# Performance work log

Hardware: AMD Instinct MI355X
Metric: run time of the kernel (lower is better)

The kernel has to match this reference:

```python
import jax, jax.numpy as jnp
import numpy as np

HALF_HIDDEN = 64  # hidden_size // 2


def _lstm_scan(xs, W_ih, W_hh):
    # xs: [T, B, H]; returns final (h, c), each [B, half_hidden]
    B = xs.shape[1]
    h0 = jnp.zeros((B, HALF_HIDDEN), xs.dtype)
    c0 = jnp.zeros((B, HALF_HIDDEN), xs.dtype)

    def step(carry, x_t):
        h, c = carry
        gates = x_t @ W_ih.T + h @ W_hh.T          # [B, 4*hh]
        i_g, f_g, g_g, o_g = jnp.split(gates, 4, axis=1)
        c_new = jax.nn.sigmoid(f_g) * c + jax.nn.sigmoid(i_g) * jnp.tanh(g_g)
        h_new = jax.nn.sigmoid(o_g) * jnp.tanh(c_new)
        return (h_new, c_new), None

    (h, c), _ = jax.lax.scan(step, (h0, c0), xs)
    return h, c


def setup_inputs() -> dict:
    key = jax.random.key(0)
    ks = jax.random.split(key, 8)
    B, T, V, H, HH = 1024, 512, 128, 128, HALF_HIDDEN
    scale = 0.1
    return {
        "x": jax.random.randint(ks[0], (B, T), 0, V, dtype=jnp.int32),
        "lengths": jax.random.randint(ks[1], (B,), 1, T, dtype=jnp.int32),
        "emb": jax.random.normal(ks[2], (V, H), jnp.float32) * scale,
        "W_ih_f": jax.random.normal(ks[3], (4 * HH, H), jnp.float32) * scale,
        "W_hh_f": jax.random.normal(ks[4], (4 * HH, HH), jnp.float32) * scale,
        "W_ih_b": jax.random.normal(ks[5], (4 * HH, H), jnp.float32) * scale,
        "W_hh_b": jax.random.normal(ks[6], (4 * HH, HH), jnp.float32) * scale,
        "W_fc": jax.random.normal(ks[7], (V, H), jnp.float32) * scale,
        "b_fc": jnp.zeros((V,), jnp.float32),
    }


def reference(x, lengths, emb, W_ih_f, W_hh_f, W_ih_b, W_hh_b, W_fc, b_fc):
    # embedding lookup: [B, T, H] -> time-major [T, B, H]
    embedded = emb[x]
    xs = jnp.transpose(embedded, (1, 0, 2))
    h_f, _ = _lstm_scan(xs, W_ih_f, W_hh_f)            # forward direction
    h_b, _ = _lstm_scan(xs[::-1], W_ih_b, W_hh_b)      # backward direction
    hidden_cat = jnp.concatenate([h_f, h_b], axis=1)   # [B, hidden]
    return hidden_cat @ W_fc.T + b_fc                  # [B, vocab]
```

## Files before the change

kernel.cpp:

```cpp
#include <hip/hip_runtime.h>
#include <hip/hip_bf16.h>


#define T_STEPS 512
#define BATCH   1024
#define VOCAB   128
#define HID     128
#define HH      64
#define NG      256
#define MB      4
#define XPITCH  520

#define L2E  1.4426950408889634f
#define L2E2 2.8853900817779268f

typedef __attribute__((ext_vector_type(8))) short bf16x8;
typedef __attribute__((ext_vector_type(4))) float f32x4;
typedef unsigned int  u32;
typedef unsigned short u16;

__device__ __forceinline__ float sigmoid_f(float x) {
    return __builtin_amdgcn_rcpf(1.0f + __builtin_amdgcn_exp2f(-x * L2E));
}
__device__ __forceinline__ float tanh_f(float x) {
    return 1.0f - 2.0f * __builtin_amdgcn_rcpf(1.0f + __builtin_amdgcn_exp2f(x * L2E2));
}
__device__ __forceinline__ u16 f2bf_rne(float f) {
    u32 u = __builtin_bit_cast(u32, f);
    u += 0x7FFFu + ((u >> 16) & 1u);
    return (u16)(u >> 16);
}
__device__ __forceinline__ void barrier_lgkm() {
    asm volatile("s_waitcnt lgkmcnt(0)\n\ts_barrier" ::: "memory");
}

__global__ __launch_bounds__(256) void build_tab_kernel(
    const float* __restrict__ emb,
    const float* __restrict__ W_ih_f,
    const float* __restrict__ W_ih_b,
    const float* __restrict__ W_hh_f,
    const float* __restrict__ W_hh_b,
    float* __restrict__ tab3,
    u16*   __restrict__ whh_bf)
{
    int v = blockIdx.x, d = blockIdx.y, tid = threadIdx.x;
    int j = tid >> 2, g = tid & 3;
    int gr = g * HH + j;
    const float* W = d ? W_ih_b : W_ih_f;
    const float4* e4 = (const float4*)(emb + v * HID);
    const float4* w4 = (const float4*)(W + gr * HID);
    float acc = 0.0f;
#pragma unroll
    for (int k = 0; k < HID / 4; ++k) {
        float4 e = e4[k]; float4 w = w4[k];
        acc += e.x * w.x + e.y * w.y + e.z * w.z + e.w * w.w;
    }
    tab3[(d * VOCAB + v) * NG + j * 4 + g] = acc;

    if (tid < 128) {
        const float* Whh = d ? W_hh_b : W_hh_f;
        int idx = v * 128 + tid;
        whh_bf[d * NG * HH + idx] = f2bf_rne(Whh[idx]);
    }
}

__global__ __launch_bounds__(256, 2) void lstm_rec_kernel(
    const int*  __restrict__ x,
    const u16*  __restrict__ whh_bf,
    const float* __restrict__ tab3,
    float* __restrict__ hfin)
{
    __shared__ __align__(16) u32 xsT[MB][XPITCH];
    __shared__ __align__(16) u16 hbuf[2][MB][80];

    const int tid  = threadIdx.x;
    const int lane = tid & 63;
    const int wave = tid >> 6;
    const int quad = lane >> 4;
    const int m    = lane & 15;
    const int dir    = blockIdx.y;
    const int b_base = blockIdx.x * MB;

    for (int i = tid; i < MB * T_STEPS; i += 256) {
        int bl = i >> 9, t = i & (T_STEPS - 1);
        int ts = dir ? (T_STEPS - 1 - t) : t;
        xsT[bl][ts] = ((u32)x[(b_base + bl) * T_STEPS + t]) << 10;
    }
    if (tid < MB * 8)
        xsT[tid >> 3][T_STEPS + (tid & 7)] = 0;
    for (int i = tid; i < (int)(sizeof(hbuf) / 4); i += 256)
        ((u32*)hbuf)[i] = 0;

    const u16* WB = whh_bf + dir * NG * HH;
    bf16x8 Bg[4][2];
#pragma unroll
    for (int g = 0; g < 4; ++g)
#pragma unroll
        for (int kc = 0; kc < 2; ++kc)
            Bg[g][kc] = *(const bf16x8*)(WB + (g * HH + wave * 16 + m) * HH
                                            + kc * 32 + quad * 8);

    const char* tabB = (const char*)tab3 + (size_t)dir * VOCAB * NG * 4;
    const u32 joff = (u32)(wave * 16 + m) * 16u;
    const int aoff = (m >> 2) * 80 + quad * 8;
    const int woff = quad * 80 + wave * 16 + m;

    const f32x4 z4 = {0.f, 0.f, 0.f, 0.f};
    float cc = 0.f, hcur = 0.f;

    __syncthreads();

    int4 qA = *(const int4*)&xsT[quad][0];
    int4 qB = *(const int4*)&xsT[quad][4];
    float4 X0 = *(const float4*)(tabB + (u32)qA.x + joff);
    float4 X1;

    auto stepf = [&](int p, const float4 Xc, float4& Xn, u32 e) {
        __builtin_amdgcn_s_setprio(1);
        const u16* rh = &hbuf[p][0][0];
        u16* wh = &hbuf[p ^ 1][0][0];
        bf16x8 Ah0 = *(const bf16x8*)(rh + aoff);
        bf16x8 Ah1 = *(const bf16x8*)(rh + aoff + 32);

        Xn = *(const float4*)(tabB + e + joff);

        f32x4 aI = __builtin_amdgcn_mfma_f32_16x16x32_bf16(Ah0, Bg[0][0], z4, 0, 0, 0);
        f32x4 aF = __builtin_amdgcn_mfma_f32_16x16x32_bf16(Ah0, Bg[1][0], z4, 0, 0, 0);
        f32x4 aG = __builtin_amdgcn_mfma_f32_16x16x32_bf16(Ah0, Bg[2][0], z4, 0, 0, 0);
        f32x4 aO = __builtin_amdgcn_mfma_f32_16x16x32_bf16(Ah0, Bg[3][0], z4, 0, 0, 0);
        aI = __builtin_amdgcn_mfma_f32_16x16x32_bf16(Ah1, Bg[0][1], aI, 0, 0, 0);
        aF = __builtin_amdgcn_mfma_f32_16x16x32_bf16(Ah1, Bg[1][1], aF, 0, 0, 0);
        aG = __builtin_amdgcn_mfma_f32_16x16x32_bf16(Ah1, Bg[2][1], aG, 0, 0, 0);
        aO = __builtin_amdgcn_mfma_f32_16x16x32_bf16(Ah1, Bg[3][1], aO, 0, 0, 0);

        float gi = aI[0] + Xc.x;
        float gf = aF[0] + Xc.y;
        float gg = aG[0] + Xc.z;
        float go = aO[0] + Xc.w;
        __builtin_amdgcn_s_setprio(0);

        cc   = sigmoid_f(gf) * cc + sigmoid_f(gi) * tanh_f(gg);
        hcur = sigmoid_f(go) * tanh_f(cc);

        u32 hb;
        asm("v_cvt_pk_bf16_f32 %0, %1, %2" : "=v"(hb) : "v"(hcur), "v"(hcur));
        wh[woff] = (u16)hb;

        barrier_lgkm();
    };

    for (int kk = 0; kk < T_STEPS / 8; ++kk) {
        stepf(0, X0, X1, (u32)qA.y);
        stepf(1, X1, X0, (u32)qA.z);
        stepf(0, X0, X1, (u32)qA.w);
        qA = *(const int4*)&xsT[quad][8 * kk + 8];
        stepf(1, X1, X0, (u32)qB.x);
        stepf(0, X0, X1, (u32)qB.y);
        stepf(1, X1, X0, (u32)qB.z);
        stepf(0, X0, X1, (u32)qB.w);
        qB = *(const int4*)&xsT[quad][8 * kk + 12];
        stepf(1, X1, X0, (u32)qA.x);
    }

    hfin[(dir * BATCH + b_base + quad) * HH + wave * 16 + m] = hcur;
}

__global__ __launch_bounds__(256) void fc_kernel(
    const float* __restrict__ hfin,
    const float* __restrict__ W_fc,
    const float* __restrict__ b_fc,
    float* __restrict__ out)
{
    __shared__ float wfc[HID * 129];
    __shared__ float hid[8][HID];
    const int tid = threadIdx.x;
    const int b0  = blockIdx.x * 8;

    for (int i = tid; i < HID * HID; i += 256) {
        int r = i >> 7, c = i & 127;
        wfc[r * 129 + c] = W_fc[i];
    }
    for (int i = tid; i < 8 * HID; i += 256) {
        int bb = i >> 7, v = i & 127;
        hid[bb][v] = (v < HH) ? hfin[(0 * BATCH + b0 + bb) * HH + v]
                              : hfin[(1 * BATCH + b0 + bb) * HH + (v - HH)];
    }
    __syncthreads();

    const int v  = tid & 127;
    const int bs = (tid >> 7) * 4;
    const float bias = b_fc[v];
    const float* wrow = wfc + v * 129;
#pragma unroll
    for (int r = 0; r < 4; ++r) {
        const float* h = hid[bs + r];
        float acc = bias;
#pragma unroll
        for (int k = 0; k < HID; k += 4) {
            acc += wrow[k]     * h[k]     + wrow[k + 1] * h[k + 1]
                 + wrow[k + 2] * h[k + 2] + wrow[k + 3] * h[k + 3];
        }
        out[(b0 + bs + r) * HID + v] = acc;
    }
}

extern "C" void kernel_launch(void* const* d_in, const int* in_sizes, int n_in,
                              void* d_out, int out_size, void* d_ws, size_t ws_size,
                              hipStream_t stream) {
    const int*   x      = (const int*)d_in[0];
    const float* emb    = (const float*)d_in[2];
    const float* W_ih_f = (const float*)d_in[3];
    const float* W_hh_f = (const float*)d_in[4];
    const float* W_ih_b = (const float*)d_in[5];
    const float* W_hh_b = (const float*)d_in[6];
    const float* W_fc   = (const float*)d_in[7];
    const float* b_fc   = (const float*)d_in[8];
    float* out = (float*)d_out;

    float* tab3   = (float*)d_ws;
    u16*   whh_bf = (u16*)(tab3 + 2 * VOCAB * NG);
    float* hfin   = (float*)(whh_bf + 2 * NG * HH);

    build_tab_kernel<<<dim3(VOCAB, 2), 256, 0, stream>>>(
        emb, W_ih_f, W_ih_b, W_hh_f, W_hh_b, tab3, whh_bf);
    lstm_rec_kernel<<<dim3(BATCH / MB, 2), 256, 0, stream>>>(x, whh_bf, tab3, hfin);
    fc_kernel<<<dim3(BATCH / 8), 256, 0, stream>>>(hfin, W_fc, b_fc, out);
}
```

Before: 214.4 us.

## Make each wave own whole batch rows and drop per-step block barriers

Restructures the LSTM recurrence so each wave holds all 64 hidden units for its own batch rows. Each wave computes the full 4x64 gate matrix with replicated W_hh fragments and rebuilds its MFMA A operand from register state via DPP swaps and ds_bpermute. This removes the LDS hidden-state double buffer and the workgroup barrier on every timestep, and doubles batch rows per block to 8. The cost is 4x more MFMA work per wave (mostly redundant, since only 16 rows are live), far more registers for B fragments (occupancy drops to 1 block per SIMD group), and half the blocks.

```diff
diff --git a/kernel.cpp b/kernel.cpp
--- a/kernel.cpp
+++ b/kernel.cpp
@@ -8,7 +8,6 @@
 #define HID     128
 #define HH      64
 #define NG      256
-#define MB      4
 #define XPITCH  520
 
 #define L2E  1.4426950408889634f
@@ -16,6 +15,7 @@
 
 typedef __attribute__((ext_vector_type(8))) short bf16x8;
 typedef __attribute__((ext_vector_type(4))) float f32x4;
+typedef __attribute__((ext_vector_type(4))) int   i32x4;
 typedef unsigned int  u32;
 typedef unsigned short u16;
 
@@ -30,8 +30,10 @@
     u += 0x7FFFu + ((u >> 16) & 1u);
     return (u16)(u >> 16);
 }
-__device__ __forceinline__ void barrier_lgkm() {
-    asm volatile("s_waitcnt lgkmcnt(0)\n\ts_barrier" ::: "memory");
+__device__ __forceinline__ float dpp_swap1(float v) {
+    int i = __builtin_bit_cast(int, v);
+    i = __builtin_amdgcn_mov_dpp(i, 0xB1, 0xF, 0xF, true);
+    return __builtin_bit_cast(float, i);
 }
 
 __global__ __launch_bounds__(256) void build_tab_kernel(
@@ -64,105 +66,130 @@
     }
 }
 
-__global__ __launch_bounds__(256, 2) void lstm_rec_kernel(
+__global__ __launch_bounds__(256, 1) void lstm_rec_kernel(
     const int*  __restrict__ x,
     const u16*  __restrict__ whh_bf,
     const float* __restrict__ tab3,
     float* __restrict__ hfin)
 {
-    __shared__ __align__(16) u32 xsT[MB][XPITCH];
-    __shared__ __align__(16) u16 hbuf[2][MB][80];
+    __shared__ __align__(16) u32 xsT[8][XPITCH];
 
     const int tid  = threadIdx.x;
     const int lane = tid & 63;
     const int wave = tid >> 6;
-    const int quad = lane >> 4;
+    const int q    = lane >> 4;
     const int m    = lane & 15;
     const int dir    = blockIdx.y;
-    const int b_base = blockIdx.x * MB;
-
-    for (int i = tid; i < MB * T_STEPS; i += 256) {
+    const int b_base = blockIdx.x * 8;
+
+    for (int i = tid; i < 8 * T_STEPS; i += 256) {
         int bl = i >> 9, t = i & (T_STEPS - 1);
         int ts = dir ? (T_STEPS - 1 - t) : t;
         xsT[bl][ts] = ((u32)x[(b_base + bl) * T_STEPS + t]) << 10;
     }
-    if (tid < MB * 8)
+    if (tid < 64)
         xsT[tid >> 3][T_STEPS + (tid & 7)] = 0;
-    for (int i = tid; i < (int)(sizeof(hbuf) / 4); i += 256)
-        ((u32*)hbuf)[i] = 0;
 
     const u16* WB = whh_bf + dir * NG * HH;
-    bf16x8 Bg[4][2];
+    bf16x8 Bg[4][4][2];
 #pragma unroll
     for (int g = 0; g < 4; ++g)
 #pragma unroll
-        for (int kc = 0; kc < 2; ++kc)
-            Bg[g][kc] = *(const bf16x8*)(WB + (g * HH + wave * 16 + m) * HH
-                                            + kc * 32 + quad * 8);
+        for (int n = 0; n < 4; ++n)
+#pragma unroll
+            for (int c = 0; c < 2; ++c)
+                Bg[g][n][c] = *(const bf16x8*)(WB + (g * 64 + n * 16 + m) * HH
+                                                  + c * 32 + q * 8);
 
     const char* tabB = (const char*)tab3 + (size_t)dir * VOCAB * NG * 4;
-    const u32 joff = (u32)(wave * 16 + m) * 16u;
-    const int aoff = (m >> 2) * 80 + quad * 8;
-    const int woff = quad * 80 + wave * 16 + m;
+    const int r     = lane >> 5;
+    const int j0    = lane & 31;
+    const u32 joff  = (u32)j0 << 4;
+    const int myrow = wave * 2 + r;
+    const int addrB = ((m >> 3) << 7) | (q << 5);
 
     const f32x4 z4 = {0.f, 0.f, 0.f, 0.f};
-    float cc = 0.f, hcur = 0.f;
+    float cc0 = 0.f, cc1 = 0.f, h0 = 0.f, h1 = 0.f;
 
     __syncthreads();
 
-    int4 qA = *(const int4*)&xsT[quad][0];
-    int4 qB = *(const int4*)&xsT[quad][4];
-    float4 X0 = *(const float4*)(tabB + (u32)qA.x + joff);
-    float4 X1;
-
-    auto stepf = [&](int p, const float4 Xc, float4& Xn, u32 e) {
-        __builtin_amdgcn_s_setprio(1);
-        const u16* rh = &hbuf[p][0][0];
-        u16* wh = &hbuf[p ^ 1][0][0];
-        bf16x8 Ah0 = *(const bf16x8*)(rh + aoff);
-        bf16x8 Ah1 = *(const bf16x8*)(rh + aoff + 32);
-
-        Xn = *(const float4*)(tabB + e + joff);
-
-        f32x4 aI = __builtin_amdgcn_mfma_f32_16x16x32_bf16(Ah0, Bg[0][0], z4, 0, 0, 0);
-        f32x4 aF = __builtin_amdgcn_mfma_f32_16x16x32_bf16(Ah0, Bg[1][0], z4, 0, 0, 0);
-        f32x4 aG = __builtin_amdgcn_mfma_f32_16x16x32_bf16(Ah0, Bg[2][0], z4, 0, 0, 0);
-        f32x4 aO = __builtin_amdgcn_mfma_f32_16x16x32_bf16(Ah0, Bg[3][0], z4, 0, 0, 0);
-        aI = __builtin_amdgcn_mfma_f32_16x16x32_bf16(Ah1, Bg[0][1], aI, 0, 0, 0);
-        aF = __builtin_amdgcn_mfma_f32_16x16x32_bf16(Ah1, Bg[1][1], aF, 0, 0, 0);
-        aG = __builtin_amdgcn_mfma_f32_16x16x32_bf16(Ah1, Bg[2][1], aG, 0, 0, 0);
-        aO = __builtin_amdgcn_mfma_f32_16x16x32_bf16(Ah1, Bg[3][1], aO, 0, 0, 0);
-
-        float gi = aI[0] + Xc.x;
-        float gf = aF[0] + Xc.y;
-        float gg = aG[0] + Xc.z;
-        float go = aO[0] + Xc.w;
-        __builtin_amdgcn_s_setprio(0);
-
-        cc   = sigmoid_f(gf) * cc + sigmoid_f(gi) * tanh_f(gg);
-        hcur = sigmoid_f(go) * tanh_f(cc);
-
-        u32 hb;
-        asm("v_cvt_pk_bf16_f32 %0, %1, %2" : "=v"(hb) : "v"(hcur), "v"(hcur));
-        wh[woff] = (u16)hb;
-
-        barrier_lgkm();
+    int4 qA = *(const int4*)&xsT[myrow][0];
+    int4 qB = *(const int4*)&xsT[myrow][4];
+    float4 XA0 = *(const float4*)(tabB + (u32)qA.x + joff);
+    float4 XA1 = *(const float4*)(tabB + (u32)qA.x + joff + 512);
+    float4 XB0, XB1;
+
+    auto stepf = [&](const float4 Xc0, const float4 Xc1,
+                     float4& Xn0, float4& Xn1, u32 e) {
+        float h0n = dpp_swap1(h0);
+        float h1n = dpp_swap1(h1);
+        u32 P0, P1;
+        asm("v_cvt_pk_bf16_f32 %0, %1, %2" : "=v"(P0) : "v"(h0), "v"(h0n));
+        asm("v_cvt_pk_bf16_f32 %0, %1, %2" : "=v"(P1) : "v"(h1), "v"(h1n));
+        int a0 = __builtin_amdgcn_ds_bpermute(addrB,      __builtin_bit_cast(int, P0));
+        int a1 = __builtin_amdgcn_ds_bpermute(addrB + 8,  __builtin_bit_cast(int, P0));
+        int a2 = __builtin_amdgcn_ds_bpermute(addrB + 16, __builtin_bit_cast(int, P0));
+        int a3 = __builtin_amdgcn_ds_bpermute(addrB + 24, __builtin_bit_cast(int, P0));
+        int b0 = __builtin_amdgcn_ds_bpermute(addrB,      __builtin_bit_cast(int, P1));
+        int b1 = __builtin_amdgcn_ds_bpermute(addrB + 8,  __builtin_bit_cast(int, P1));
+        int b2 = __builtin_amdgcn_ds_bpermute(addrB + 16, __builtin_bit_cast(int, P1));
+        int b3 = __builtin_amdgcn_ds_bpermute(addrB + 24, __builtin_bit_cast(int, P1));
+        i32x4 va = {a0, a1, a2, a3};
+        i32x4 vb = {b0, b1, b2, b3};
+        bf16x8 A0 = __builtin_bit_cast(bf16x8, va);
+        bf16x8 A1 = __builtin_bit_cast(bf16x8, vb);
+
+        Xn0 = *(const float4*)(tabB + e + joff);
+        Xn1 = *(const float4*)(tabB + e + joff + 512);
+
+        f32x4 acc[4][4];
+#pragma unroll
+        for (int g = 0; g < 4; ++g)
+#pragma unroll
+            for (int n = 0; n < 4; ++n)
+                acc[g][n] = __builtin_amdgcn_mfma_f32_16x16x32_bf16(
+                    A0, Bg[g][n][0], z4, 0, 0, 0);
+#pragma unroll
+        for (int g = 0; g < 4; ++g)
+#pragma unroll
+            for (int n = 0; n < 4; ++n)
+                acc[g][n] = __builtin_amdgcn_mfma_f32_16x16x32_bf16(
+                    A1, Bg[g][n][1], acc[g][n], 0, 0, 0);
+
+        const bool s = (q & 1);
+        float gi0 = (s ? acc[0][1][0] : acc[0][0][0]) + Xc0.x;
+        float gf0 = (s ? acc[1][1][0] : acc[1][0][0]) + Xc0.y;
+        float gg0 = (s ? acc[2][1][0] : acc[2][0][0]) + Xc0.z;
+        float go0 = (s ? acc[3][1][0] : acc[3][0][0]) + Xc0.w;
+        float gi1 = (s ? acc[0][3][0] : acc[0][2][0]) + Xc1.x;
+        float gf1 = (s ? acc[1][3][0] : acc[1][2][0]) + Xc1.y;
+        float gg1 = (s ? acc[2][3][0] : acc[2][2][0]) + Xc1.z;
+        float go1 = (s ? acc[3][3][0] : acc[3][2][0]) + Xc1.w;
+
+        cc0 = sigmoid_f(gf0) * cc0 + sigmoid_f(gi0) * tanh_f(gg0);
+        h0  = sigmoid_f(go0) * tanh_f(cc0);
+        cc1 = sigmoid_f(gf1) * cc1 + sigmoid_f(gi1) * tanh_f(gg1);
+        h1  = sigmoid_f(go1) * tanh_f(cc1);
     };
 
     for (int kk = 0; kk < T_STEPS / 8; ++kk) {
-        stepf(0, X0, X1, (u32)qA.y);
-        stepf(1, X1, X0, (u32)qA.z);
-        stepf(0, X0, X1, (u32)qA.w);
-        qA = *(const int4*)&xsT[quad][8 * kk + 8];
-        stepf(1, X1, X0, (u32)qB.x);
-        stepf(0, X0, X1, (u32)qB.y);
-        stepf(1, X1, X0, (u32)qB.z);
-        stepf(0, X0, X1, (u32)qB.w);
-        qB = *(const int4*)&xsT[quad][8 * kk + 12];
-        stepf(1, X1, X0, (u32)qA.x);
-    }
-
-    hfin[(dir * BATCH + b_base + quad) * HH + wave * 16 + m] = hcur;
+        stepf(XA0, XA1, XB0, XB1, (u32)qA.y);
+        stepf(XB0, XB1, XA0, XA1, (u32)qA.z);
+        stepf(XA0, XA1, XB0, XB1, (u32)qA.w);
+        qA = *(const int4*)&xsT[myrow][8 * kk + 8];
+        stepf(XB0, XB1, XA0, XA1, (u32)qB.x);
+        stepf(XA0, XA1, XB0, XB1, (u32)qB.y);
+        stepf(XB0, XB1, XA0, XA1, (u32)qB.z);
+        stepf(XA0, XA1, XB0, XB1, (u32)qB.w);
+        qB = *(const int4*)&xsT[myrow][8 * kk + 12];
+        stepf(XB0, XB1, XA0, XA1, (u32)qA.x);
+    }
+
+    {
+        float* dst = hfin + ((size_t)dir * BATCH + b_base + myrow) * HH;
+        dst[j0]      = h0;
+        dst[j0 + 32] = h1;
+    }
 }
 
 __global__ __launch_bounds__(256) void fc_kernel(
@@ -223,6 +250,6 @@
 
     build_tab_kernel<<<dim3(VOCAB, 2), 256, 0, stream>>>(
         emb, W_ih_f, W_ih_b, W_hh_f, W_hh_b, tab3, whh_bf);
-    lstm_rec_kernel<<<dim3(BATCH / MB, 2), 256, 0, stream>>>(x, whh_bf, tab3, hfin);
+    lstm_rec_kernel<<<dim3(BATCH / 8, 2), 256, 0, stream>>>(x, whh_bf, tab3, hfin);
     fc_kernel<<<dim3(BATCH / 8), 256, 0, stream>>>(hfin, W_fc, b_fc, out);
 }
```

Measured after the change: 344.1 us. 60.5% more time.

## Halve batch rows per block and give each wave 32 hidden units

Applied to the files above, without the earlier changes.

Reduces the recurrent block from four waves over four batch rows to two waves over two batch rows. Each wave now computes two 16-column MFMA tiles per gate, covering 32 hidden units, and selects its result by lane group. The intent is a cheaper two-wave barrier and more independent blocks to hide latency. The cost is double the MFMAs per wave per step on the serial recurrence path, and more redundant rows in the MFMA A operand.

```diff
diff --git a/kernel.cpp b/kernel.cpp
--- a/kernel.cpp
+++ b/kernel.cpp
@@ -8,7 +8,7 @@
 #define HID     128
 #define HH      64
 #define NG      256
-#define MB      4
+#define MB      2
 #define XPITCH  520
 
 #define L2E  1.4426950408889634f
@@ -64,7 +64,7 @@
     }
 }
 
-__global__ __launch_bounds__(256, 2) void lstm_rec_kernel(
+__global__ __launch_bounds__(128, 2) void lstm_rec_kernel(
     const int*  __restrict__ x,
     const u16*  __restrict__ whh_bf,
     const float* __restrict__ tab3,
@@ -76,42 +76,46 @@
     const int tid  = threadIdx.x;
     const int lane = tid & 63;
     const int wave = tid >> 6;
-    const int quad = lane >> 4;
+    const int q    = lane >> 4;
     const int m    = lane & 15;
     const int dir    = blockIdx.y;
     const int b_base = blockIdx.x * MB;
 
-    for (int i = tid; i < MB * T_STEPS; i += 256) {
+    for (int i = tid; i < MB * T_STEPS; i += 128) {
         int bl = i >> 9, t = i & (T_STEPS - 1);
         int ts = dir ? (T_STEPS - 1 - t) : t;
         xsT[bl][ts] = ((u32)x[(b_base + bl) * T_STEPS + t]) << 10;
     }
     if (tid < MB * 8)
         xsT[tid >> 3][T_STEPS + (tid & 7)] = 0;
-    for (int i = tid; i < (int)(sizeof(hbuf) / 4); i += 256)
+    for (int i = tid; i < (int)(sizeof(hbuf) / 4); i += 128)
         ((u32*)hbuf)[i] = 0;
 
     const u16* WB = whh_bf + dir * NG * HH;
-    bf16x8 Bg[4][2];
+    bf16x8 Bg[4][2][2];
 #pragma unroll
     for (int g = 0; g < 4; ++g)
 #pragma unroll
-        for (int kc = 0; kc < 2; ++kc)
-            Bg[g][kc] = *(const bf16x8*)(WB + (g * HH + wave * 16 + m) * HH
-                                            + kc * 32 + quad * 8);
+        for (int n = 0; n < 2; ++n)
+#pragma unroll
+            for (int c = 0; c < 2; ++c)
+                Bg[g][n][c] = *(const bf16x8*)(
+                    WB + (g * 64 + wave * 32 + n * 16 + m) * HH + c * 32 + q * 8);
 
     const char* tabB = (const char*)tab3 + (size_t)dir * VOCAB * NG * 4;
-    const u32 joff = (u32)(wave * 16 + m) * 16u;
-    const int aoff = (m >> 2) * 80 + quad * 8;
-    const int woff = quad * 80 + wave * 16 + m;
+    const int r    = q >> 1;
+    const int jj   = wave * 32 + (q & 1) * 16 + m;
+    const u32 joff = (u32)jj << 4;
+    const int aoff = (m >> 3) * 80 + q * 8;
+    const int woff = r * 80 + jj;
 
     const f32x4 z4 = {0.f, 0.f, 0.f, 0.f};
     float cc = 0.f, hcur = 0.f;
 
     __syncthreads();
 
-    int4 qA = *(const int4*)&xsT[quad][0];
-    int4 qB = *(const int4*)&xsT[quad][4];
+    int4 qA = *(const int4*)&xsT[r][0];
+    int4 qB = *(const int4*)&xsT[r][4];
     float4 X0 = *(const float4*)(tabB + (u32)qA.x + joff);
     float4 X1;
 
@@ -124,19 +128,25 @@
 
         Xn = *(const float4*)(tabB + e + joff);
 
-        f32x4 aI = __builtin_amdgcn_mfma_f32_16x16x32_bf16(Ah0, Bg[0][0], z4, 0, 0, 0);
-        f32x4 aF = __builtin_amdgcn_mfma_f32_16x16x32_bf16(Ah0, Bg[1][0], z4, 0, 0, 0);
-        f32x4 aG = __builtin_amdgcn_mfma_f32_16x16x32_bf16(Ah0, Bg[2][0], z4, 0, 0, 0);
-        f32x4 aO = __builtin_amdgcn_mfma_f32_16x16x32_bf16(Ah0, Bg[3][0], z4, 0, 0, 0);
-        aI = __builtin_amdgcn_mfma_f32_16x16x32_bf16(Ah1, Bg[0][1], aI, 0, 0, 0);
-        aF = __builtin_amdgcn_mfma_f32_16x16x32_bf16(Ah1, Bg[1][1], aF, 0, 0, 0);
-        aG = __builtin_amdgcn_mfma_f32_16x16x32_bf16(Ah1, Bg[2][1], aG, 0, 0, 0);
-        aO = __builtin_amdgcn_mfma_f32_16x16x32_bf16(Ah1, Bg[3][1], aO, 0, 0, 0);
-
-        float gi = aI[0] + Xc.x;
-        float gf = aF[0] + Xc.y;
-        float gg = aG[0] + Xc.z;
-        float go = aO[0] + Xc.w;
+        f32x4 acc[4][2];
+#pragma unroll
+        for (int g = 0; g < 4; ++g)
+#pragma unroll
+            for (int n = 0; n < 2; ++n)
+                acc[g][n] = __builtin_amdgcn_mfma_f32_16x16x32_bf16(
+                    Ah0, Bg[g][n][0], z4, 0, 0, 0);
+#pragma unroll
+        for (int g = 0; g < 4; ++g)
+#pragma unroll
+            for (int n = 0; n < 2; ++n)
+                acc[g][n] = __builtin_amdgcn_mfma_f32_16x16x32_bf16(
+                    Ah1, Bg[g][n][1], acc[g][n], 0, 0, 0);
+
+        const bool s = (q & 1);
+        float gi = (s ? acc[0][1][0] : acc[0][0][0]) + Xc.x;
+        float gf = (s ? acc[1][1][0] : acc[1][0][0]) + Xc.y;
+        float gg = (s ? acc[2][1][0] : acc[2][0][0]) + Xc.z;
+        float go = (s ? acc[3][1][0] : acc[3][0][0]) + Xc.w;
         __builtin_amdgcn_s_setprio(0);
 
         cc   = sigmoid_f(gf) * cc + sigmoid_f(gi) * tanh_f(gg);
@@ -153,16 +163,16 @@
         stepf(0, X0, X1, (u32)qA.y);
         stepf(1, X1, X0, (u32)qA.z);
         stepf(0, X0, X1, (u32)qA.w);
-        qA = *(const int4*)&xsT[quad][8 * kk + 8];
+        qA = *(const int4*)&xsT[r][8 * kk + 8];
         stepf(1, X1, X0, (u32)qB.x);
         stepf(0, X0, X1, (u32)qB.y);
         stepf(1, X1, X0, (u32)qB.z);
         stepf(0, X0, X1, (u32)qB.w);
-        qB = *(const int4*)&xsT[quad][8 * kk + 12];
+        qB = *(const int4*)&xsT[r][8 * kk + 12];
         stepf(1, X1, X0, (u32)qA.x);
     }
 
-    hfin[(dir * BATCH + b_base + quad) * HH + wave * 16 + m] = hcur;
+    hfin[(dir * BATCH + b_base + r) * HH + jj] = hcur;
 }
 
 __global__ __launch_bounds__(256) void fc_kernel(
@@ -223,6 +233,6 @@
 
     build_tab_kernel<<<dim3(VOCAB, 2), 256, 0, stream>>>(
         emb, W_ih_f, W_ih_b, W_hh_f, W_hh_b, tab3, whh_bf);
-    lstm_rec_kernel<<<dim3(BATCH / MB, 2), 256, 0, stream>>>(x, whh_bf, tab3, hfin);
+    lstm_rec_kernel<<<dim3(BATCH / MB, 2), 128, 0, stream>>>(x, whh_bf, tab3, hfin);
     fc_kernel<<<dim3(BATCH / 8), 256, 0, stream>>>(hfin, W_fc, b_fc, out);
 }
```

After: 278.4 us. 29.9% more time.

## Fuse final FC projection into LSTM kernel via atomic partial sums, drop setprio

Applied to the files above, without the earlier changes.

Removes the separate fc_kernel. Each recurrence block writes its final hidden state to shared memory and computes its direction's half of the output projection, which it adds into the output with atomicAdd. The output is zeroed with a memset first, and only the forward-direction blocks add the bias. The s_setprio hints around the MFMA section are also removed. This saves one kernel launch and the hfin round trip through global memory, at the cost of an extra memset, atomics, and fp32 addition order that is no longer deterministic.

```diff
diff --git a/kernel.cpp b/kernel.cpp
--- a/kernel.cpp
+++ b/kernel.cpp
@@ -68,7 +68,9 @@
     const int*  __restrict__ x,
     const u16*  __restrict__ whh_bf,
     const float* __restrict__ tab3,
-    float* __restrict__ hfin)
+    const float* __restrict__ W_fc,
+    const float* __restrict__ b_fc,
+    float* __restrict__ out)
 {
     __shared__ __align__(16) u32 xsT[MB][XPITCH];
     __shared__ __align__(16) u16 hbuf[2][MB][80];
@@ -116,7 +118,6 @@
     float4 X1;
 
     auto stepf = [&](int p, const float4 Xc, float4& Xn, u32 e) {
-        __builtin_amdgcn_s_setprio(1);
         const u16* rh = &hbuf[p][0][0];
         u16* wh = &hbuf[p ^ 1][0][0];
         bf16x8 Ah0 = *(const bf16x8*)(rh + aoff);
@@ -137,7 +138,6 @@
         float gf = aF[0] + Xc.y;
         float gg = aG[0] + Xc.z;
         float go = aO[0] + Xc.w;
-        __builtin_amdgcn_s_setprio(0);
 
         cc   = sigmoid_f(gf) * cc + sigmoid_f(gi) * tanh_f(gg);
         hcur = sigmoid_f(go) * tanh_f(cc);
@@ -162,45 +162,34 @@
         stepf(1, X1, X0, (u32)qA.x);
     }
 
-    hfin[(dir * BATCH + b_base + quad) * HH + wave * 16 + m] = hcur;
-}
-
-__global__ __launch_bounds__(256) void fc_kernel(
-    const float* __restrict__ hfin,
-    const float* __restrict__ W_fc,
-    const float* __restrict__ b_fc,
-    float* __restrict__ out)
-{
-    __shared__ float wfc[HID * 129];
-    __shared__ float hid[8][HID];
-    const int tid = threadIdx.x;
-    const int b0  = blockIdx.x * 8;
-
-    for (int i = tid; i < HID * HID; i += 256) {
-        int r = i >> 7, c = i & 127;
-        wfc[r * 129 + c] = W_fc[i];
-    }
-    for (int i = tid; i < 8 * HID; i += 256) {
-        int bb = i >> 7, v = i & 127;
-        hid[bb][v] = (v < HH) ? hfin[(0 * BATCH + b0 + bb) * HH + v]
-                              : hfin[(1 * BATCH + b0 + bb) * HH + (v - HH)];
-    }
+    float* hs = (float*)&xsT[0][0];
+    hs[quad * HH + wave * 16 + m] = hcur;
     __syncthreads();
 
-    const int v  = tid & 127;
-    const int bs = (tid >> 7) * 4;
-    const float bias = b_fc[v];
-    const float* wrow = wfc + v * 129;
-#pragma unroll
-    for (int r = 0; r < 4; ++r) {
-        const float* h = hid[bs + r];
-        float acc = bias;
-#pragma unroll
-        for (int k = 0; k < HID; k += 4) {
-            acc += wrow[k]     * h[k]     + wrow[k + 1] * h[k + 1]
-                 + wrow[k + 2] * h[k + 2] + wrow[k + 3] * h[k + 3];
+    {
+        const int v  = tid & 127;
+        const int rp = tid >> 7;
+        const int r0 = 2 * rp, r1 = 2 * rp + 1;
+        const float* wv = W_fc + v * HID + dir * HH;
+        const float4* w4 = (const float4*)wv;
+        const float4* h4a = (const float4*)(hs + r0 * HH);
+        const float4* h4b = (const float4*)(hs + r1 * HH);
+        float acc0 = 0.f, acc1 = 0.f;
+#pragma unroll
+        for (int k = 0; k < HH / 4; ++k) {
+            float4 w = w4[k];
+            float4 a = h4a[k];
+            float4 b = h4b[k];
+            acc0 += w.x * a.x + w.y * a.y + w.z * a.z + w.w * a.w;
+            acc1 += w.x * b.x + w.y * b.y + w.z * b.z + w.w * b.w;
         }
-        out[(b0 + bs + r) * HID + v] = acc;
+        if (dir == 0) {
+            float bias = b_fc[v];
+            acc0 += bias;
+            acc1 += bias;
+        }
+        atomicAdd(&out[(b_base + r0) * HID + v], acc0);
+        atomicAdd(&out[(b_base + r1) * HID + v], acc1);
     }
 }
 
@@ -219,10 +208,10 @@
 
     float* tab3   = (float*)d_ws;
     u16*   whh_bf = (u16*)(tab3 + 2 * VOCAB * NG);
-    float* hfin   = (float*)(whh_bf + 2 * NG * HH);
-
+
+    hipMemsetAsync(out, 0, out_size, stream);
     build_tab_kernel<<<dim3(VOCAB, 2), 256, 0, stream>>>(
         emb, W_ih_f, W_ih_b, W_hh_f, W_hh_b, tab3, whh_bf);
-    lstm_rec_kernel<<<dim3(BATCH / MB, 2), 256, 0, stream>>>(x, whh_bf, tab3, hfin);
-    fc_kernel<<<dim3(BATCH / 8), 256, 0, stream>>>(hfin, W_fc, b_fc, out);
-}
+    lstm_rec_kernel<<<dim3(BATCH / MB, 2), 256, 0, stream>>>(
+        x, whh_bf, tab3, W_fc, b_fc, out);
+}
```

Result: no change. 213.8 us (-0.3%).
